# Performance work log

Measured on AMD Instinct MI355X. Metric: run time of the kernel, lower is better.

The kernel has to match this reference:

```python
import jax, jax.numpy as jnp
import numpy as np

DEPTH = 4  # init kwarg 'depth'
H = 256   # init kwarg 'hidden_size'
ATOM_FDIM, BOND_FDIM = 35, 5


def _build_graph(rng, N, E):
    src = rng.integers(0, N, E).astype(np.int32)
    dst = rng.integers(0, N, E).astype(np.int32)
    # line graph (backtracking=False): lg edge e1 -> e2 iff dst[e1]==src[e2] and src[e1]!=dst[e2]
    indeg = np.bincount(dst, minlength=N)
    idx_sorted = np.argsort(dst, kind='stable')          # edge ids grouped by dst node
    ptr = np.concatenate([[0], np.cumsum(indeg)]).astype(np.int64)
    counts = indeg[src]                                   # in-edges of src[e] feed edge e
    total = int(counts.sum())
    lg_dst = np.repeat(np.arange(E, dtype=np.int64), counts)
    cum = np.cumsum(counts) - counts
    within = np.arange(total) - np.repeat(cum, counts)
    lg_src = idx_sorted[np.repeat(ptr[src], counts) + within]
    keep = src[lg_src] != dst[lg_dst]                     # drop backtracking pairs
    return src, dst, lg_src[keep].astype(np.int32), lg_dst[keep].astype(np.int32)


def setup_inputs() -> dict:
    rng = np.random.default_rng(0)
    N, E, Et, K, G = 50000, 200000, 100000, 50000, 2000
    src, dst, lg_src, lg_dst = _build_graph(rng, N, E)
    graph_ids = ((np.arange(N, dtype=np.int64) * G) // N).astype(np.int32)
    f32 = lambda *s: rng.standard_normal(s).astype(np.float32)
    return {
        'x_nodes': jnp.asarray(f32(N, ATOM_FDIM)),
        'x_edges': jnp.asarray(rng.random((E, BOND_FDIM)).astype(np.float32)),
        'tree_m': jnp.asarray(f32(Et, H) * 0.1),
        'W_i': jnp.asarray(f32(ATOM_FDIM + BOND_FDIM, H) * 0.05),
        'W_h': jnp.asarray(f32(H, H) * 0.05),
        'W_o': jnp.asarray(f32(ATOM_FDIM + H, H) * 0.05),
        'b_o': jnp.asarray(f32(H) * 0.05),
        'edge_src': jnp.asarray(src),
        'edge_dst': jnp.asarray(dst),
        'lg_src': jnp.asarray(lg_src),
        'lg_dst': jnp.asarray(lg_dst),
        'tgt_nodes': jnp.asarray(rng.integers(0, N, K).astype(np.int32)),
        'tree_eid': jnp.asarray(rng.integers(0, Et, K).astype(np.int32)),
        'graph_ids': jnp.asarray(graph_ids),
        'n_graphs': G,
    }


def reference(x_nodes, x_edges, tree_m, W_i, W_h, W_o, b_o,
              edge_src, edge_dst, lg_src, lg_dst, tgt_nodes, tree_eid,
              graph_ids, n_graphs):
    N = x_nodes.shape[0]
    E = x_edges.shape[0]
    # edge input features: [src atom feats | bond feats] @ W_i (no bias)
    msg_input = jnp.concatenate([x_nodes[edge_src], x_edges], axis=1) @ W_i  # [E,H]
    msg = jax.nn.relu(msg_input)
    # tree message alignment: scatter-add tree edge messages onto cand nodes
    node_alpha = jnp.zeros((N, msg.shape[1]), msg.dtype).at[tgt_nodes].add(tree_m[tree_eid])
    edge_alpha = node_alpha[edge_src]  # apply_edges: alpha = src alpha
    # loopy BP over the line graph
    for _ in range(DEPTH - 1):
        accum = jax.ops.segment_sum(msg[lg_src], lg_dst, num_segments=E)  # [E,H]
        msg = jax.nn.relu(msg_input + (accum + edge_alpha) @ W_h)
    # gather: m = sum of incoming edge messages per node
    m = jax.ops.segment_sum(msg, edge_dst, num_segments=N)  # [N,H]
    h = jax.nn.relu(jnp.concatenate([x_nodes, m + node_alpha], axis=1) @ W_o + b_o)
    # mean_nodes per candidate graph
    sums = jax.ops.segment_sum(h, graph_ids, num_segments=n_graphs)
    cnt = jax.ops.segment_sum(jnp.ones((N, 1), h.dtype), graph_ids, num_segments=n_graphs)
    return sums / jnp.maximum(cnt, 1.0)
```

## Files before the change

### kernel.cpp

```cpp
#include <hip/hip_runtime.h>
#include <stdint.h>

typedef unsigned short u16;
typedef __attribute__((ext_vector_type(8))) short bf16x8;
typedef __attribute__((ext_vector_type(4))) float f32x4;

#define HD 256
#define AST 264
#define GRP 64
#define CORR_CAP 2048

static __device__ __forceinline__ float b2f(u16 x){
  union{float f; unsigned u;} v; v.u = ((unsigned)x)<<16; return v.f;
}
static __device__ __forceinline__ u16 f2b(float f){
  union{float f; unsigned u;} v; v.f = f;
  unsigned r = v.u + 0x7fffu + ((v.u>>16)&1u);
  return (u16)(r>>16);
}
static __device__ __forceinline__ void racc2(float* a, uint2 iv, uint2 vv){
  float t0 = b2f((u16)iv.x)       + b2f((u16)vv.x);
  float t1 = b2f((u16)(iv.x>>16)) + b2f((u16)(vv.x>>16));
  float t2 = b2f((u16)iv.y)       + b2f((u16)vv.y);
  float t3 = b2f((u16)(iv.y>>16)) + b2f((u16)(vv.y>>16));
  a[0] += t0>0.f?t0:0.f; a[1] += t1>0.f?t1:0.f;
  a[2] += t2>0.f?t2:0.f; a[3] += t3>0.f?t3:0.f;
}
static __device__ __forceinline__ void racc1(float* a, uint2 iv){
  float t0 = b2f((u16)iv.x), t1 = b2f((u16)(iv.x>>16));
  float t2 = b2f((u16)iv.y), t3 = b2f((u16)(iv.y>>16));
  a[0] += t0>0.f?t0:0.f; a[1] += t1>0.f?t1:0.f;
  a[2] += t2>0.f?t2:0.f; a[3] += t3>0.f?t3:0.f;
}

static __device__ __forceinline__ void prep_frag_body(const float* __restrict__ W,
    int k0, int kmax, u16* __restrict__ out, int lb, int tid){
  int g = lb*256 + tid;
  int i = g & 7, l = (g>>3)&63, t = g>>9;
  int nj = t & 15, ks = t >> 4;
  int n = nj*16 + (l&15);
  int k = ks*32 + (l>>4)*8 + i;
  float v = (k < kmax) ? W[(size_t)(k0+k)*HD + n] : 0.f;
  out[g] = f2b(v);
}
__global__ void k_prep_all(const float* __restrict__ Wi, const float* __restrict__ Wh,
                           const float* __restrict__ Wo, const float* __restrict__ xn,
                           u16* __restrict__ BT_P, u16* __restrict__ BT_Wh,
                           u16* __restrict__ BT_Ra, u16* __restrict__ BT_Wob,
                           u16* __restrict__ xnf, int* __restrict__ deg2,
                           int N, int zb){
  int b = blockIdx.x, tid = threadIdx.x;
  if (b < 64){ prep_frag_body(Wi, 0, 35, BT_P, b, tid); return; }
  b -= 64;
  if (b < 256){ prep_frag_body(Wh, 0, 256, BT_Wh, b, tid); return; }
  b -= 256;
  if (b < 64){ prep_frag_body(Wo, 0, 35, BT_Ra, b, tid); return; }
  b -= 64;
  if (b < 256){ prep_frag_body(Wo, 35, 256, BT_Wob, b, tid); return; }
  b -= 256;
  if (b < zb){
    int i = b*256 + tid;
    if (i < 2*N+1) deg2[i] = 0;
    return;
  }
  b -= zb;
  {
    long long g = (long long)b*256 + tid;
    int v2 = (int)(g >> 6), c = (int)(g & 63);
    if (v2 >= N) return;
    float v = (c < 35) ? xn[(size_t)v2*35 + c] : 0.f;
    xnf[g] = f2b(v);
  }
}

__global__ void k_hist2(const int* __restrict__ tgt, const int* __restrict__ edst,
                        int* __restrict__ deg2, int K, int E, int N, int kgrid){
  int b = blockIdx.x;
  if (b < kgrid){
    int i = b*256 + threadIdx.x;
    if (i < K) atomicAdd(&deg2[tgt[i]], 1);
  } else {
    int i = (b-kgrid)*256 + threadIdx.x;
    if (i < E) atomicAdd(&deg2[N + edst[i]], 1);
  }
}

__global__ void k_scan_p1(const int* __restrict__ deg, int n, int* __restrict__ bsum){
  int i = blockIdx.x*256 + threadIdx.x;
  int v = (i < n) ? deg[i] : 0;
  #pragma unroll
  for (int o=32; o>0; o>>=1) v += __shfl_down(v, o);
  __shared__ int w[4];
  if ((threadIdx.x&63)==0) w[threadIdx.x>>6] = v;
  __syncthreads();
  if (threadIdx.x==0) bsum[blockIdx.x] = w[0]+w[1]+w[2]+w[3];
}
__global__ __launch_bounds__(1024) void k_scan_p2(int* __restrict__ bsum, int nb,
                                                  int* __restrict__ total_dst){
  __shared__ int sm[1024];
  int t = threadIdx.x;
  int v = (t < nb) ? bsum[t] : 0;
  sm[t] = v; __syncthreads();
  for (int o=1; o<1024; o<<=1){
    int u = (t>=o) ? sm[t-o] : 0;
    __syncthreads();
    sm[t] += u;
    __syncthreads();
  }
  if (t < nb) bsum[t] = sm[t] - v;
  if (t == 1023 && total_dst) *total_dst = sm[1023];
}
__global__ void k_scan_p3(const int* __restrict__ deg, const int* __restrict__ bsum, int n,
                          int* __restrict__ start, int* __restrict__ cursor){
  int t = threadIdx.x;
  int i = blockIdx.x*256 + t;
  int v = (i < n) ? deg[i] : 0;
  __shared__ int sm[256];
  sm[t] = v; __syncthreads();
  for (int o=1; o<256; o<<=1){
    int u = (t>=o) ? sm[t-o] : 0;
    __syncthreads();
    sm[t] += u;
    __syncthreads();
  }
  int ex = sm[t] - v + bsum[blockIdx.x];
  if (i < n){ start[i] = ex; cursor[i] = ex; }
}

__global__ void k_fill2(const int* __restrict__ tgt, const int* __restrict__ teid,
                        const int* __restrict__ edst, int* __restrict__ cursor2,
                        int* __restrict__ bucket2, int K, int E, int N, int kgrid){
  int b = blockIdx.x;
  if (b < kgrid){
    int i = b*256 + threadIdx.x;
    if (i >= K) return;
    int pos = atomicAdd(&cursor2[tgt[i]], 1);
    bucket2[pos] = teid[i];
  } else {
    int e = (b-kgrid)*256 + threadIdx.x;
    if (e >= E) return;
    int pos = atomicAdd(&cursor2[N + edst[e]], 1);
    bucket2[pos] = e;
  }
}

__global__ void k_perm_xep(const int* __restrict__ bucket2, int K,
                           const int* __restrict__ esrc, const int* __restrict__ edst,
                           const float* __restrict__ xe,
                           int* __restrict__ esrc_p, int* __restrict__ edst_p,
                           float* __restrict__ xep, int E){
  int e = blockIdx.x*256 + threadIdx.x;
  if (e >= E) return;
  int o = bucket2[K + e];
  esrc_p[e] = esrc[o];
  edst_p[e] = edst[o];
  #pragma unroll
  for (int k=0;k<5;k++) xep[(size_t)e*5+k] = xe[(size_t)o*5+k];
}

__global__ void k_alpha_pairs(const float* __restrict__ tree_m,
                              const int* __restrict__ start2, const int* __restrict__ bucket2,
                              u16* __restrict__ alpha16,
                              const int* __restrict__ esrc_p, const int* __restrict__ edst_p,
                              int* __restrict__ npairs, int2* __restrict__ pairs,
                              int N, int E, int K, int agrid){
  int b = blockIdx.x;
  if (b < agrid){
    int v = (int)(((long long)b*256 + threadIdx.x)>>6);
    int l = threadIdx.x & 63;
    if (v >= N) return;
    int s = start2[v], e2 = start2[v+1];
    float a0=0.f,a1=0.f,a2=0.f,a3=0.f;
    for (int j=s;j<e2;j++){
      float4 tv = *(const float4*)(tree_m + (size_t)bucket2[j]*HD + l*4);
      a0 += tv.x; a1 += tv.y; a2 += tv.z; a3 += tv.w;
    }
    ushort4 o; o.x=f2b(a0); o.y=f2b(a1); o.z=f2b(a2); o.w=f2b(a3);
    *(ushort4*)(alpha16 + (size_t)v*HD + l*4) = o;
  } else {
    int e = (b-agrid)*256 + threadIdx.x;
    if (e >= E) return;
    int u = esrc_p[e], v = edst_p[e];
    int s = start2[N+u] - K, t = start2[N+u+1] - K;
    for (int ep=s; ep<t; ep++){
      if (esrc_p[ep] == v){
        int pos = atomicAdd(npairs, 1);
        if (pos < CORR_CAP) pairs[pos] = (int2){e, ep};
      }
    }
  }
}

__global__ __launch_bounds__(512, 4) void k_pr2(
    const u16* __restrict__ xnf, const u16* __restrict__ BT_P,
    const u16* __restrict__ BT_Ra, u16* __restrict__ P, u16* __restrict__ R, int M)
{
  const int tid = threadIdx.x;
  const int w = tid>>6, l = tid&63;
  const int lr = l&15, lq = l>>4;
  const int nrb = (M+15)>>4;
  bf16x8 BP0[2], BP1[2], BR0[2], BR1[2];
  #pragma unroll
  for (int ks=0; ks<2; ks++){
    BP0[ks] = *(const bf16x8*)(BT_P  + (size_t)((ks*16 + w*2  )*512) + l*8);
    BP1[ks] = *(const bf16x8*)(BT_P  + (size_t)((ks*16 + w*2+1)*512) + l*8);
    BR0[ks] = *(const bf16x8*)(BT_Ra + (size_t)((ks*16 + w*2  )*512) + l*8);
    BR1[ks] = *(const bf16x8*)(BT_Ra + (size_t)((ks*16 + w*2+1)*512) + l*8);
  }
  const int c0 = w*32 + lr, c1 = w*32 + 16 + lr;
  for (int rb = blockIdx.x; rb < nrb; rb += gridDim.x){
    int r = rb*16 + lr; int rc = min(r, M-1);
    const u16* fr = xnf + (size_t)rc*64 + lq*8;
    bf16x8 a0 = *(const bf16x8*)(fr);
    bf16x8 a1 = *(const bf16x8*)(fr + 32);
    f32x4 p0={0.f,0.f,0.f,0.f}, p1={0.f,0.f,0.f,0.f};
    f32x4 r0={0.f,0.f,0.f,0.f}, r1={0.f,0.f,0.f,0.f};
    p0 = __builtin_amdgcn_mfma_f32_16x16x32_bf16(a0, BP0[0], p0, 0,0,0);
    p0 = __builtin_amdgcn_mfma_f32_16x16x32_bf16(a1, BP0[1], p0, 0,0,0);
    p1 = __builtin_amdgcn_mfma_f32_16x16x32_bf16(a0, BP1[0], p1, 0,0,0);
    p1 = __builtin_amdgcn_mfma_f32_16x16x32_bf16(a1, BP1[1], p1, 0,0,0);
    r0 = __builtin_amdgcn_mfma_f32_16x16x32_bf16(a0, BR0[0], r0, 0,0,0);
    r0 = __builtin_amdgcn_mfma_f32_16x16x32_bf16(a1, BR0[1], r0, 0,0,0);
    r1 = __builtin_amdgcn_mfma_f32_16x16x32_bf16(a0, BR1[0], r1, 0,0,0);
    r1 = __builtin_amdgcn_mfma_f32_16x16x32_bf16(a1, BR1[1], r1, 0,0,0);
    #pragma unroll
    for (int reg=0; reg<4; reg++){
      int gm = rb*16 + lq*4 + reg;
      if (gm < M){
        P[(size_t)gm*HD + c0] = f2b(p0[reg]);
        P[(size_t)gm*HD + c1] = f2b(p1[reg]);
        R[(size_t)gm*HD + c0] = f2b(r0[reg]);
        R[(size_t)gm*HD + c1] = f2b(r1[reg]);
      }
    }
  }
}

__global__ __launch_bounds__(256, 8) void k_build_I(
    const u16* __restrict__ P, const float* __restrict__ xep,
    const int* __restrict__ esrc_p, const float* __restrict__ Wi,
    u16* __restrict__ I, int E)
{
  const int l = threadIdx.x & 63;
  const int wid = (blockIdx.x*256 + threadIdx.x) >> 6;
  const int nw = gridDim.x*4;
  float wq[5][4];
  #pragma unroll
  for (int k=0;k<5;k++){
    float4 t = *(const float4*)(Wi + (size_t)(35+k)*HD + l*4);
    wq[k][0]=t.x; wq[k][1]=t.y; wq[k][2]=t.z; wq[k][3]=t.w;
  }
  for (int e = wid; e < E; e += nw){
    int s = esrc_p[e];
    const float* xp = xep + (size_t)e*5;
    float x0=xp[0], x1=xp[1], x2=xp[2], x3=xp[3], x4=xp[4];
    uint2 uv = *(const uint2*)(P + (size_t)s*HD + l*4);
    float v[4] = { b2f((u16)uv.x), b2f((u16)(uv.x>>16)),
                   b2f((u16)uv.y), b2f((u16)(uv.y>>16)) };
    #pragma unroll
    for (int j=0;j<4;j++)
      v[j] += x0*wq[0][j] + x1*wq[1][j] + x2*wq[2][j] + x3*wq[3][j] + x4*wq[4][j];
    ushort4 o; o.x=f2b(v[0]); o.y=f2b(v[1]); o.z=f2b(v[2]); o.w=f2b(v[3]);
    *(ushort4*)(I + (size_t)e*HD + l*4) = o;
  }
}

__global__ void k_msgA0(const u16* __restrict__ I, const int2* __restrict__ pairs,
                        const int* __restrict__ npairs_p, float* __restrict__ msgA){
  int np = *npairs_p; if (np > CORR_CAP) np = CORR_CAP;
  int t = threadIdx.x;
  for (int p = blockIdx.x; p < np; p += gridDim.x){
    int ep = pairs[p].y;
    float v = b2f(I[(size_t)ep*HD + t]);
    msgA[(size_t)p*HD + t] = v > 0.f ? v : 0.f;
  }
}

__global__ __launch_bounds__(512, 4) void k_bp(
    const u16* __restrict__ I, const u16* __restrict__ Vprev,
    const u16* __restrict__ alpha16, const int* __restrict__ start_d, int KBIAS,
    const int* __restrict__ esrc_p, const u16* __restrict__ BTf,
    const u16* __restrict__ Radd, const float* __restrict__ bias,
    u16* __restrict__ Sout, u16* __restrict__ Vout, float* __restrict__ hout,
    int N, int mode)
{
  __shared__ u16 A_lds[GRP][AST];
  const int tid = threadIdx.x;
  const int w = tid>>6, l = tid&63;
  const int lr = l&15, lq = l>>4;
  const int ngrp = (N+GRP-1)/GRP;

  bf16x8 B0[8], B1[8];
  #pragma unroll
  for (int ks=0; ks<8; ks++){
    B0[ks] = *(const bf16x8*)(BTf + (size_t)((ks*16 + w*2  )*512) + l*8);
    B1[ks] = *(const bf16x8*)(BTf + (size_t)((ks*16 + w*2+1)*512) + l*8);
  }
  const int c0 = w*32 + lr, c1 = w*32 + 16 + lr;
  float b0 = 0.f, b1 = 0.f;
  if (mode == 1){ b0 = bias[c0]; b1 = bias[c1]; }

  for (int grp = blockIdx.x; grp < ngrp; grp += gridDim.x){
    const int vb = grp*GRP;
    #pragma unroll 2
    for (int hh=0; hh<8; hh++){
      int v = vb + w*8 + hh;
      float a[4] = {0.f,0.f,0.f,0.f};
      if (v < N){
        uint2 av = *(const uint2*)(alpha16 + (size_t)v*HD + l*4);
        a[0]=b2f((u16)av.x); a[1]=b2f((u16)(av.x>>16));
        a[2]=b2f((u16)av.y); a[3]=b2f((u16)(av.y>>16));
        int s = start_d[v] - KBIAS, e2 = start_d[v+1] - KBIAS;
        int cnt = e2 - s;
        const u16* Ir0 = I + (size_t)s*HD + l*4;
        if (Vprev){
          const int* sp = esrc_p + s;
          int done = 0;
          while (done < cnt){
            int m = min(64, cnt - done);
            int idx = (l < m) ? sp[done + l] : 0;
            int j = 0;
            for (; j+2 <= m; j+=2){
              int s0 = __shfl(idx, j), s1 = __shfl(idx, j+1);
              uint2 i0 = *(const uint2*)(Ir0 + (size_t)(done+j  )*HD);
              uint2 i1 = *(const uint2*)(Ir0 + (size_t)(done+j+1)*HD);
              uint2 v0 = *(const uint2*)(Vprev + (size_t)s0*HD + l*4);
              uint2 v1 = *(const uint2*)(Vprev + (size_t)s1*HD + l*4);
              racc2(a, i0, v0); racc2(a, i1, v1);
            }
            if (j < m){
              int s0 = __shfl(idx, j);
              uint2 i0 = *(const uint2*)(Ir0 + (size_t)(done+j)*HD);
              uint2 v0 = *(const uint2*)(Vprev + (size_t)s0*HD + l*4);
              racc2(a, i0, v0);
            }
            done += m;
          }
        } else {
          int j = 0;
          for (; j+2 <= cnt; j+=2){
            uint2 i0 = *(const uint2*)(Ir0 + (size_t)j*HD);
            uint2 i1 = *(const uint2*)(Ir0 + (size_t)(j+1)*HD);
            racc1(a, i0); racc1(a, i1);
          }
          if (j < cnt) racc1(a, *(const uint2*)(Ir0 + (size_t)j*HD));
        }
      }
      ushort4 o; o.x=f2b(a[0]); o.y=f2b(a[1]); o.z=f2b(a[2]); o.w=f2b(a[3]);
      if (v < N && Sout) *(ushort4*)(Sout + (size_t)v*HD + l*4) = o;
      *(ushort4*)&A_lds[w*8+hh][l*4] = o;
    }
    __syncthreads();
    #pragma unroll
    for (int t4=0; t4<4; t4++){
      f32x4 acc0 = (f32x4){0.f,0.f,0.f,0.f};
      f32x4 acc1 = (f32x4){0.f,0.f,0.f,0.f};
      const u16* Ar = &A_lds[t4*16 + lr][0];
      #pragma unroll
      for (int ks=0; ks<8; ks++){
        bf16x8 af = *(const bf16x8*)(Ar + ks*32 + lq*8);
        acc0 = __builtin_amdgcn_mfma_f32_16x16x32_bf16(af, B0[ks], acc0, 0,0,0);
        acc1 = __builtin_amdgcn_mfma_f32_16x16x32_bf16(af, B1[ks], acc1, 0,0,0);
      }
      #pragma unroll
      for (int reg=0; reg<4; reg++){
        int gm = vb + t4*16 + lq*4 + reg;
        if (gm < N){
          if (mode == 1){
            float v0 = acc0[reg] + b2f(Radd[(size_t)gm*HD + c0]) + b0;
            float v1 = acc1[reg] + b2f(Radd[(size_t)gm*HD + c1]) + b1;
            hout[(size_t)gm*HD + c0] = v0 > 0.f ? v0 : 0.f;
            hout[(size_t)gm*HD + c1] = v1 > 0.f ? v1 : 0.f;
          } else {
            Vout[(size_t)gm*HD + c0] = f2b(acc0[reg]);
            Vout[(size_t)gm*HD + c1] = f2b(acc1[reg]);
          }
        }
      }
    }
    __syncthreads();
  }
}

__global__ __launch_bounds__(256) void k_corr1(
    const u16* __restrict__ I, const u16* __restrict__ Vprev,
    const int* __restrict__ esrc_p,
    const int2* __restrict__ pairs, const int* __restrict__ npairs_p,
    const float* __restrict__ Wh, const float* __restrict__ msgA,
    float* __restrict__ newA, float* __restrict__ deltaS)
{
  int np = *npairs_p; if (np > CORR_CAP) np = CORR_CAP;
  int t = threadIdx.x;
  __shared__ float cs[HD];
  for (int p = blockIdx.x; p < np; p += gridDim.x){
    int e = pairs[p].x;
    bool first = true;
    for (int q=0;q<p;q++) if (pairs[q].x == e){ first=false; break; }
    __syncthreads();
    if (first){
      float c = 0.f;
      for (int q=p;q<np;q++) if (pairs[q].x == e) c += msgA[(size_t)q*HD + t];
      cs[t] = c;
    }
    __syncthreads();
    if (first){
      float a0=0.f,a1=0.f,a2=0.f,a3=0.f;
      for (int k=0;k<HD;k+=4){
        a0 += cs[k]  *Wh[(size_t)k*HD+t];
        a1 += cs[k+1]*Wh[(size_t)(k+1)*HD+t];
        a2 += cs[k+2]*Wh[(size_t)(k+2)*HD+t];
        a3 += cs[k+3]*Wh[(size_t)(k+3)*HD+t];
      }
      float corr = (a0+a1)+(a2+a3);
      int u = esrc_p[e];
      float base = b2f(I[(size_t)e*HD + t]) + b2f(Vprev[(size_t)u*HD + t]);
      float mn = base > 0.f ? base : 0.f;
      float bt = base - corr;
      float mt = bt > 0.f ? bt : 0.f;
      deltaS[(size_t)p*HD + t] = mt - mn;
      for (int q=0;q<np;q++) if (pairs[q].y == e) newA[(size_t)q*HD + t] = mt;
    }
  }
}

__global__ __launch_bounds__(256) void k_corrV(
    const int2* __restrict__ pairs, const int* __restrict__ npairs_p,
    const int* __restrict__ edst_p, const float* __restrict__ deltaS,
    float* __restrict__ msgA, const float* __restrict__ newA,
    const float* __restrict__ Wh, u16* __restrict__ Vcur)
{
  int np = *npairs_p; if (np > CORR_CAP) np = CORR_CAP;
  int t = threadIdx.x;
  __shared__ float ds[HD];
  for (int p = blockIdx.x; p < np; p += gridDim.x)
    msgA[(size_t)p*HD + t] = newA[(size_t)p*HD + t];
  for (int p = blockIdx.x; p < np; p += gridDim.x){
    int dv = edst_p[pairs[p].x];
    bool firstdv = true;
    for (int q=0;q<p;q++) if (edst_p[pairs[q].x] == dv){ firstdv=false; break; }
    __syncthreads();
    if (firstdv){
      float d = 0.f;
      for (int q=p;q<np;q++){
        if (edst_p[pairs[q].x] != dv) continue;
        bool fe = true;
        for (int r=0;r<q;r++) if (pairs[r].x == pairs[q].x){ fe=false; break; }
        if (fe) d += deltaS[(size_t)q*HD + t];
      }
      ds[t] = d;
    }
    __syncthreads();
    if (firstdv){
      float a0=0.f,a1=0.f,a2=0.f,a3=0.f;
      for (int k=0;k<HD;k+=4){
        a0 += ds[k]  *Wh[(size_t)k*HD+t];
        a1 += ds[k+1]*Wh[(size_t)(k+1)*HD+t];
        a2 += ds[k+2]*Wh[(size_t)(k+2)*HD+t];
        a3 += ds[k+3]*Wh[(size_t)(k+3)*HD+t];
      }
      float dot = (a0+a1)+(a2+a3);
      u16* vp = Vcur + (size_t)dv*HD + t;
      *vp = f2b(b2f(*vp) + dot);
    }
  }
}

__global__ __launch_bounds__(256, 1) void k_corr2(
    const int2* __restrict__ pairs, const int* __restrict__ npairs_p,
    const int* __restrict__ edst_p, const float* __restrict__ deltaS,
    float* __restrict__ msgA, const float* __restrict__ newA,
    u16* __restrict__ Scur)
{
  int np = *npairs_p; if (np > CORR_CAP) np = CORR_CAP;
  int t = threadIdx.x;
  for (int p=0; p<np; p++){
    msgA[(size_t)p*HD + t] = newA[(size_t)p*HD + t];
    int e = pairs[p].x;
    bool first = true;
    for (int q=0;q<p;q++) if (pairs[q].x == e){ first=false; break; }
    if (first){
      int dv = edst_p[e];
      u16* sp = Scur + (size_t)dv*HD + t;
      *sp = f2b(b2f(*sp) + deltaS[(size_t)p*HD + t]);
    }
    __syncthreads();
  }
}

__global__ __launch_bounds__(256) void k_corr3(
    const int2* __restrict__ pairs, const int* __restrict__ npairs_p,
    const int* __restrict__ edst_p, const u16* __restrict__ Scur,
    const float* __restrict__ Wob, const u16* __restrict__ Radd,
    const float* __restrict__ bias, float* __restrict__ hout)
{
  int np = *npairs_p; if (np > CORR_CAP) np = CORR_CAP;
  int t = threadIdx.x;
  __shared__ float sa[HD];
  for (int p = blockIdx.x; p < np; p += gridDim.x){
    int dv = edst_p[pairs[p].x];
    bool first = true;
    for (int q=0;q<p;q++) if (edst_p[pairs[q].x] == dv){ first=false; break; }
    __syncthreads();
    if (first) sa[t] = b2f(Scur[(size_t)dv*HD + t]);
    __syncthreads();
    if (first){
      float a0=0.f,a1=0.f,a2=0.f,a3=0.f;
      for (int k=0;k<HD;k+=4){
        a0 += sa[k]  *Wob[(size_t)k*HD+t];
        a1 += sa[k+1]*Wob[(size_t)(k+1)*HD+t];
        a2 += sa[k+2]*Wob[(size_t)(k+2)*HD+t];
        a3 += sa[k+3]*Wob[(size_t)(k+3)*HD+t];
      }
      float acc = (a0+a1)+(a2+a3);
      float hv = acc + b2f(Radd[(size_t)dv*HD + t]) + bias[t];
      hout[(size_t)dv*HD + t] = hv > 0.f ? hv : 0.f;
    }
  }
}

__global__ void k_graph_mean(const float* __restrict__ h, const int* __restrict__ gid,
                             int N, int G, float* __restrict__ out){
  int g = (int)(((long long)blockIdx.x*blockDim.x + threadIdx.x)>>6);
  int l = threadIdx.x & 63;
  if (g >= G) return;
  int lo=0, hi=N;
  while (lo<hi){ int mid=(lo+hi)>>1; if (gid[mid] < g) lo=mid+1; else hi=mid; }
  int b = lo;
  hi = N;
  while (lo<hi){ int mid=(lo+hi)>>1; if (gid[mid] < g+1) lo=mid+1; else hi=mid; }
  int e2 = lo;
  float a0=0.f,a1=0.f,a2=0.f,a3=0.f;
  for (int v=b; v<e2; v++){
    float4 hv = *(const float4*)(h + (size_t)v*HD + l*4);
    a0 += hv.x; a1 += hv.y; a2 += hv.z; a3 += hv.w;
  }
  int cnt = e2 - b; if (cnt < 1) cnt = 1;
  float inv = 1.0f/(float)cnt;
  float4 o; o.x=a0*inv; o.y=a1*inv; o.z=a2*inv; o.w=a3*inv;
  *(float4*)(out + (size_t)g*HD + l*4) = o;
}

extern "C" void kernel_launch(void* const* d_in, const int* in_sizes, int n_in,
                              void* d_out, int out_size, void* d_ws, size_t ws_size,
                              hipStream_t stream){
  const float* x_nodes = (const float*)d_in[0];
  const float* x_edges = (const float*)d_in[1];
  const float* tree_m  = (const float*)d_in[2];
  const float* W_i     = (const float*)d_in[3];
  const float* W_h     = (const float*)d_in[4];
  const float* W_o     = (const float*)d_in[5];
  const float* b_o     = (const float*)d_in[6];
  const int* edge_src = (const int*)d_in[7];
  const int* edge_dst = (const int*)d_in[8];
  const int* tgt      = (const int*)d_in[11];
  const int* teid     = (const int*)d_in[12];
  const int* gid      = (const int*)d_in[13];

  const int N = in_sizes[0]/35;
  const int E = in_sizes[1]/5;
  const int K = in_sizes[11];
  const int G = out_size/HD;
  const int N2 = 2*N;

  char* wsb = (char*)d_ws;
  auto align256 = [](size_t x){ return (x + 255) & ~(size_t)255; };
  size_t oI      = 0;
  size_t oSa     = oI      + align256((size_t)E*HD*2);
  size_t oVa     = oSa     + align256((size_t)N*HD*2);
  size_t oP      = oVa     + align256((size_t)N*HD*2);
  size_t oVb     = oP      + align256((size_t)N*HD*2);
  size_t oR      = oVb     + align256((size_t)N*HD*2);
  size_t oAlpha  = oR      + align256((size_t)N*HD*2);
  size_t oXnf    = oAlpha  + align256((size_t)N*HD*2);
  size_t oXep    = oXnf    + align256((size_t)N*64*2);
  size_t oBTP    = oXep    + align256((size_t)E*5*4);
  size_t oBTWh   = oBTP    + align256((size_t)2*16*512*2);
  size_t oBTRa   = oBTWh   + align256((size_t)8*16*512*2);
  size_t oBTWob  = oBTRa   + align256((size_t)2*16*512*2);
  size_t oDeg2   = oBTWob  + align256((size_t)8*16*512*2);
  size_t oStart2 = oDeg2   + align256((size_t)(N2+1)*4);
  size_t oCur2   = oStart2 + align256((size_t)(N2+1)*4);
  size_t oBuk2   = oCur2   + align256((size_t)N2*4);
  size_t oEsrcP  = oBuk2   + align256((size_t)(K+E)*4);
  size_t oEdstP  = oEsrcP  + align256((size_t)E*4);
  size_t oBsum   = oEdstP  + align256((size_t)E*4);
  size_t oPairs  = oBsum   + align256((size_t)1024*4);
  size_t oMsgA   = oPairs  + align256((size_t)CORR_CAP*8);
  size_t oNewA   = oMsgA   + align256((size_t)CORR_CAP*HD*4);
  size_t oDeltaS = oNewA   + align256((size_t)CORR_CAP*HD*4);

  u16*   I       = (u16*)(wsb + oI);
  u16*   Sa      = (u16*)(wsb + oSa);
  u16*   Va      = (u16*)(wsb + oVa);
  u16*   P       = (u16*)(wsb + oP);
  u16*   Vb      = (u16*)(wsb + oVb);
  u16*   R       = (u16*)(wsb + oR);
  u16*   alpha16 = (u16*)(wsb + oAlpha);
  u16*   xnf     = (u16*)(wsb + oXnf);
  float* xep     = (float*)(wsb + oXep);
  u16*   BT_P    = (u16*)(wsb + oBTP);
  u16*   BT_Wh   = (u16*)(wsb + oBTWh);
  u16*   BT_Ra   = (u16*)(wsb + oBTRa);
  u16*   BT_Wob  = (u16*)(wsb + oBTWob);
  int*   deg2    = (int*)(wsb + oDeg2);
  int*   npairs  = deg2 + N2;
  int*   start2  = (int*)(wsb + oStart2);
  int*   cursor2 = (int*)(wsb + oCur2);
  int*   bucket2 = (int*)(wsb + oBuk2);
  int*   esrc_p  = (int*)(wsb + oEsrcP);
  int*   edst_p  = (int*)(wsb + oEdstP);
  int*   bsum    = (int*)(wsb + oBsum);
  int2*  pairs   = (int2*)(wsb + oPairs);
  float* msgA    = (float*)(wsb + oMsgA);
  float* newA    = (float*)(wsb + oNewA);
  float* deltaS  = (float*)(wsb + oDeltaS);
  float* hbuf    = (float*)(wsb + oP);

  const int egrid256 = (E+255)/256;
  const int kgrid256 = (K+255)/256;
  const int nb2      = (N2+255)/256;
  const int zb       = (N2+1+255)/256;
  const int xnfb     = (int)(((size_t)N*64+255)/256);
  const int agrid    = (N+3)/4;
  const int ngrp     = (N+GRP-1)/GRP;

  k_prep_all<<<640+zb+xnfb, 256, 0, stream>>>(W_i, W_h, W_o, x_nodes,
                                              BT_P, BT_Wh, BT_Ra, BT_Wob,
                                              xnf, deg2, N, zb);
  k_hist2<<<kgrid256+egrid256, 256, 0, stream>>>(tgt, edge_dst, deg2, K, E, N, kgrid256);
  k_scan_p1<<<nb2, 256, 0, stream>>>(deg2, N2, bsum);
  k_scan_p2<<<1, 1024, 0, stream>>>(bsum, nb2, start2 + N2);
  k_scan_p3<<<nb2, 256, 0, stream>>>(deg2, bsum, N2, start2, cursor2);
  k_fill2<<<kgrid256+egrid256, 256, 0, stream>>>(tgt, teid, edge_dst, cursor2, bucket2,
                                                 K, E, N, kgrid256);
  k_perm_xep<<<egrid256, 256, 0, stream>>>(bucket2, K, edge_src, edge_dst, x_edges,
                                           esrc_p, edst_p, xep, E);
  k_alpha_pairs<<<agrid+egrid256, 256, 0, stream>>>(tree_m, start2, bucket2, alpha16,
                                                    esrc_p, edst_p, npairs, pairs,
                                                    N, E, K, agrid);
  k_pr2<<<512, 512, 0, stream>>>(xnf, BT_P, BT_Ra, P, R, N);
  k_build_I<<<2048, 256, 0, stream>>>(P, xep, esrc_p, W_i, I, E);
  k_msgA0<<<64, 256, 0, stream>>>(I, pairs, npairs, msgA);

  const float* Wob = W_o + 35*HD;
  const int* start_d = start2 + N;

  k_bp<<<ngrp, 512, 0, stream>>>(I, (const u16*)0, alpha16, start_d, K, esrc_p, BT_Wh,
                                 (const u16*)0, (const float*)0,
                                 (u16*)0, Va, (float*)0, N, 0);
  k_bp<<<ngrp, 512, 0, stream>>>(I, Va, alpha16, start_d, K, esrc_p, BT_Wh,
                                 (const u16*)0, (const float*)0,
                                 (u16*)0, Vb, (float*)0, N, 0);
  k_corr1<<<64, 256, 0, stream>>>(I, Va, esrc_p, pairs, npairs, W_h, msgA, newA, deltaS);
  k_corrV<<<64, 256, 0, stream>>>(pairs, npairs, edst_p, deltaS, msgA, newA, W_h, Vb);
  k_bp<<<ngrp, 512, 0, stream>>>(I, Vb, alpha16, start_d, K, esrc_p, BT_Wh,
                                 (const u16*)0, (const float*)0,
                                 (u16*)0, Va, (float*)0, N, 0);
  k_corr1<<<64, 256, 0, stream>>>(I, Vb, esrc_p, pairs, npairs, W_h, msgA, newA, deltaS);
  k_corrV<<<64, 256, 0, stream>>>(pairs, npairs, edst_p, deltaS, msgA, newA, W_h, Va);
  k_bp<<<ngrp, 512, 0, stream>>>(I, Va, alpha16, start_d, K, esrc_p, BT_Wob,
                                 R, b_o, Sa, (u16*)0, hbuf, N, 1);
  k_corr1<<<64, 256, 0, stream>>>(I, Va, esrc_p, pairs, npairs, W_h, msgA, newA, deltaS);
  k_corr2<<<1, 256, 0, stream>>>(pairs, npairs, edst_p, deltaS, msgA, newA, Sa);
  k_corr3<<<64, 256, 0, stream>>>(pairs, npairs, edst_p, Sa, Wob, R, b_o, hbuf);

  k_graph_mean<<<(G+3)/4, 256, 0, stream>>>(hbuf, gid, N, G, (float*)d_out);
}
```

Baseline: 623.6 us.

## Stage k_bp MFMA outputs through LDS for coalesced stores, halve group size

The k_bp kernel now writes MFMA results into an LDS staging buffer and then emits coalesced 16-byte row stores to Vout/hout, replacing scattered 2- and 4-byte per-element global writes. The node group per block shrinks from 64 to 32 rows, and the gather loops are unrolled by 4 to keep more loads in flight. This adds extra LDS use and two more __syncthreads per 16-row tile. The smaller group also means the B fragments held in registers are reused over fewer rows.

```diff
diff --git a/kernel.cpp b/kernel.cpp
--- a/kernel.cpp
+++ b/kernel.cpp
@@ -7,7 +7,7 @@
 
 #define HD 256
 #define AST 264
-#define GRP 64
+#define GRP 32
 #define CORR_CAP 2048
 
 static __device__ __forceinline__ float b2f(u16 x){
@@ -285,6 +285,7 @@
     int N, int mode)
 {
   __shared__ u16 A_lds[GRP][AST];
+  __shared__ char out_stage[16*HD*4];
   const int tid = threadIdx.x;
   const int w = tid>>6, l = tid&63;
   const int lr = l&15, lq = l>>4;
@@ -302,9 +303,8 @@
 
   for (int grp = blockIdx.x; grp < ngrp; grp += gridDim.x){
     const int vb = grp*GRP;
-    #pragma unroll 2
-    for (int hh=0; hh<8; hh++){
-      int v = vb + w*8 + hh;
+    for (int hh=0; hh<4; hh++){
+      int v = vb + w*4 + hh;
       float a[4] = {0.f,0.f,0.f,0.f};
       if (v < N){
         uint2 av = *(const uint2*)(alpha16 + (size_t)v*HD + l*4);
@@ -320,15 +320,21 @@
             int m = min(64, cnt - done);
             int idx = (l < m) ? sp[done + l] : 0;
             int j = 0;
-            for (; j+2 <= m; j+=2){
-              int s0 = __shfl(idx, j), s1 = __shfl(idx, j+1);
+            for (; j+4 <= m; j+=4){
+              int s0 = __shfl(idx, j),   s1 = __shfl(idx, j+1);
+              int s2 = __shfl(idx, j+2), s3 = __shfl(idx, j+3);
               uint2 i0 = *(const uint2*)(Ir0 + (size_t)(done+j  )*HD);
               uint2 i1 = *(const uint2*)(Ir0 + (size_t)(done+j+1)*HD);
+              uint2 i2 = *(const uint2*)(Ir0 + (size_t)(done+j+2)*HD);
+              uint2 i3 = *(const uint2*)(Ir0 + (size_t)(done+j+3)*HD);
               uint2 v0 = *(const uint2*)(Vprev + (size_t)s0*HD + l*4);
               uint2 v1 = *(const uint2*)(Vprev + (size_t)s1*HD + l*4);
+              uint2 v2 = *(const uint2*)(Vprev + (size_t)s2*HD + l*4);
+              uint2 v3 = *(const uint2*)(Vprev + (size_t)s3*HD + l*4);
               racc2(a, i0, v0); racc2(a, i1, v1);
+              racc2(a, i2, v2); racc2(a, i3, v3);
             }
-            if (j < m){
+            for (; j < m; j++){
               int s0 = __shfl(idx, j);
               uint2 i0 = *(const uint2*)(Ir0 + (size_t)(done+j)*HD);
               uint2 v0 = *(const uint2*)(Vprev + (size_t)s0*HD + l*4);
@@ -338,21 +344,23 @@
           }
         } else {
           int j = 0;
-          for (; j+2 <= cnt; j+=2){
+          for (; j+4 <= cnt; j+=4){
             uint2 i0 = *(const uint2*)(Ir0 + (size_t)j*HD);
             uint2 i1 = *(const uint2*)(Ir0 + (size_t)(j+1)*HD);
-            racc1(a, i0); racc1(a, i1);
+            uint2 i2 = *(const uint2*)(Ir0 + (size_t)(j+2)*HD);
+            uint2 i3 = *(const uint2*)(Ir0 + (size_t)(j+3)*HD);
+            racc1(a, i0); racc1(a, i1); racc1(a, i2); racc1(a, i3);
           }
-          if (j < cnt) racc1(a, *(const uint2*)(Ir0 + (size_t)j*HD));
+          for (; j < cnt; j++) racc1(a, *(const uint2*)(Ir0 + (size_t)j*HD));
         }
       }
       ushort4 o; o.x=f2b(a[0]); o.y=f2b(a[1]); o.z=f2b(a[2]); o.w=f2b(a[3]);
       if (v < N && Sout) *(ushort4*)(Sout + (size_t)v*HD + l*4) = o;
-      *(ushort4*)&A_lds[w*8+hh][l*4] = o;
+      *(ushort4*)&A_lds[w*4+hh][l*4] = o;
     }
     __syncthreads();
     #pragma unroll
-    for (int t4=0; t4<4; t4++){
+    for (int t4=0; t4<2; t4++){
       f32x4 acc0 = (f32x4){0.f,0.f,0.f,0.f};
       f32x4 acc1 = (f32x4){0.f,0.f,0.f,0.f};
       const u16* Ar = &A_lds[t4*16 + lr][0];
@@ -362,23 +370,48 @@
         acc0 = __builtin_amdgcn_mfma_f32_16x16x32_bf16(af, B0[ks], acc0, 0,0,0);
         acc1 = __builtin_amdgcn_mfma_f32_16x16x32_bf16(af, B1[ks], acc1, 0,0,0);
       }
-      #pragma unroll
-      for (int reg=0; reg<4; reg++){
-        int gm = vb + t4*16 + lq*4 + reg;
-        if (gm < N){
-          if (mode == 1){
-            float v0 = acc0[reg] + b2f(Radd[(size_t)gm*HD + c0]) + b0;
-            float v1 = acc1[reg] + b2f(Radd[(size_t)gm*HD + c1]) + b1;
-            hout[(size_t)gm*HD + c0] = v0 > 0.f ? v0 : 0.f;
-            hout[(size_t)gm*HD + c1] = v1 > 0.f ? v1 : 0.f;
-          } else {
-            Vout[(size_t)gm*HD + c0] = f2b(acc0[reg]);
-            Vout[(size_t)gm*HD + c1] = f2b(acc1[reg]);
+      if (mode == 1){
+        float* of = (float*)out_stage;
+        #pragma unroll
+        for (int reg=0; reg<4; reg++){
+          int gm = vb + t4*16 + lq*4 + reg;
+          float v0 = acc0[reg] + b0, v1 = acc1[reg] + b1;
+          if (gm < N){
+            v0 += b2f(Radd[(size_t)gm*HD + c0]);
+            v1 += b2f(Radd[(size_t)gm*HD + c1]);
+          }
+          of[(lq*4+reg)*HD + c0] = v0 > 0.f ? v0 : 0.f;
+          of[(lq*4+reg)*HD + c1] = v1 > 0.f ? v1 : 0.f;
+        }
+        __syncthreads();
+        {
+          int row = tid >> 5, off = (tid & 31)*8;
+          int gm = vb + t4*16 + row;
+          if (gm < N){
+            const float4* srcp = (const float4*)(of + row*HD + off);
+            float4* dstp = (float4*)(hout + (size_t)gm*HD + off);
+            dstp[0] = srcp[0]; dstp[1] = srcp[1];
           }
         }
-      }
-    }
-    __syncthreads();
+        __syncthreads();
+      } else {
+        u16* ou = (u16*)out_stage;
+        #pragma unroll
+        for (int reg=0; reg<4; reg++){
+          ou[(lq*4+reg)*HD + c0] = f2b(acc0[reg]);
+          ou[(lq*4+reg)*HD + c1] = f2b(acc1[reg]);
+        }
+        __syncthreads();
+        {
+          int row = tid >> 5, off = (tid & 31)*8;
+          int gm = vb + t4*16 + row;
+          if (gm < N){
+            *(bf16x8*)(Vout + (size_t)gm*HD + off) = *(const bf16x8*)(ou + row*HD + off);
+          }
+        }
+        __syncthreads();
+      }
+    }
   }
 }
 
```

Measured after the change: 785.8 us. 26.0% more time.
